# Performance work log

Measured on AMD Instinct MI355X. Metric: run time of the kernel, lower is better.

The kernel has to match this reference:

```python
import jax, jax.numpy as jnp
import numpy as np

D_MODEL = 1024
D_INTERNAL = 256


def setup_inputs() -> dict:
    key = jax.random.key(0)
    ks = jax.random.split(key, 10)
    s = lambda fan_in: 1.0 / np.sqrt(fan_in)
    inp = {
        "input_vecs": jax.random.normal(ks[0], (4, 2048, D_MODEL), dtype=jnp.float32),
        # Linear weights stored as (in, out) for x @ W
        "wq": jax.random.uniform(ks[1], (D_MODEL, D_INTERNAL), minval=-s(D_MODEL), maxval=s(D_MODEL), dtype=jnp.float32),
        "wk": jax.random.uniform(ks[2], (D_MODEL, D_INTERNAL), minval=-s(D_MODEL), maxval=s(D_MODEL), dtype=jnp.float32),
        "wv": jax.random.uniform(ks[3], (D_MODEL, D_MODEL), minval=-s(D_MODEL), maxval=s(D_MODEL), dtype=jnp.float32),
        "wo": jax.random.uniform(ks[4], (D_MODEL, D_MODEL), minval=-s(D_MODEL), maxval=s(D_MODEL), dtype=jnp.float32),
        "bo": jax.random.uniform(ks[5], (D_MODEL,), minval=-s(D_MODEL), maxval=s(D_MODEL), dtype=jnp.float32),
        "w1": jax.random.uniform(ks[6], (D_MODEL, D_INTERNAL), minval=-s(D_MODEL), maxval=s(D_MODEL), dtype=jnp.float32),
        "b1": jax.random.uniform(ks[7], (D_INTERNAL,), minval=-s(D_MODEL), maxval=s(D_MODEL), dtype=jnp.float32),
        "w2": jax.random.uniform(ks[8], (D_INTERNAL, D_MODEL), minval=-s(D_INTERNAL), maxval=s(D_INTERNAL), dtype=jnp.float32),
        "b2": jax.random.uniform(ks[9], (D_MODEL,), minval=-s(D_INTERNAL), maxval=s(D_INTERNAL), dtype=jnp.float32),
    }
    return inp


def reference(input_vecs, wq, wk, wv, wo, bo, w1, b1, w2, b2):
    # Single-head self-attention (causal=False default path)
    q = jnp.einsum("btd,dk->btk", input_vecs, wq)  # (B,T,d_internal)
    k = jnp.einsum("btd,dk->btk", input_vecs, wk)
    v = jnp.einsum("btd,de->bte", input_vecs, wv)  # (B,T,d_model)
    scale = 1.0 / jnp.sqrt(jnp.asarray(q.shape[-1], dtype=q.dtype))
    scores = jnp.einsum("bqk,btk->bqt", q, k) * scale  # (B,T,T)
    attn = jax.nn.softmax(scores, axis=-1)
    context = jnp.einsum("bqt,bte->bqe", attn, v)  # (B,T,d_model)
    context = jnp.einsum("bte,eo->bto", context, wo) + bo
    residual = input_vecs + context
    h = jax.nn.relu(jnp.einsum("btd,dk->btk", residual, w1) + b1)
    ff = jnp.einsum("btk,kd->btd", h, w2) + b2
    out = residual + ff
    return out, attn
```

## Files before the change

kernel.cpp:

```cpp
#include <hip/hip_runtime.h>

typedef unsigned short u16;
typedef unsigned int u32;
typedef __bf16 bf16x8 __attribute__((ext_vector_type(8)));
typedef float f32x4 __attribute__((ext_vector_type(4)));

#define MTOT 8192
#define DM 1024
#define DI 256
#define TT 2048

#define AS1 __attribute__((address_space(1)))
#define AS3 __attribute__((address_space(3)))

__device__ __forceinline__ u16 f2bf(float f) {
    u32 u = __float_as_uint(f);
    return (u16)((u + 0x7fffu + ((u >> 16) & 1u)) >> 16);
}
__device__ __forceinline__ float b2f(u16 b) {
    return __uint_as_float((u32)b << 16);
}

__device__ __forceinline__ int xcd_swizzle(int bid, int nb) {
    return (bid & 7) * (nb >> 3) + (bid >> 3);
}

__device__ __forceinline__ void transpose_tile(const float* __restrict__ in,
                                               u16* __restrict__ out, int K, int N,
                                               int bx, int by) {
    __shared__ float t[32][33];
    int n0 = bx * 32, k0 = by * 32;
    int tx = threadIdx.x & 31, ty = threadIdx.x >> 5;
    #pragma unroll
    for (int i = ty; i < 32; i += 8) t[i][tx] = in[(long)(k0 + i) * N + n0 + tx];
    __syncthreads();
    #pragma unroll
    for (int i = ty; i < 32; i += 8) out[(long)(n0 + i) * K + k0 + tx] = f2bf(t[tx][i]);
}

__device__ __forceinline__ void cvt_range(const float* __restrict__ in,
                                          u16* __restrict__ out, long n4, int b, int nb) {
    long i = (long)b * 256 + threadIdx.x;
    long stride = (long)nb * 256;
    for (; i < n4; i += stride) {
        float4 v = reinterpret_cast<const float4*>(in)[i];
        union { u16 u[4]; uint2 p; } o;
        o.u[0] = f2bf(v.x); o.u[1] = f2bf(v.y); o.u[2] = f2bf(v.z); o.u[3] = f2bf(v.w);
        reinterpret_cast<uint2*>(out)[i] = o.p;
    }
}

__global__ __launch_bounds__(256) void prep_kernel(
    const float* __restrict__ x, u16* __restrict__ Xb,
    const float* __restrict__ wq, const float* __restrict__ wk, u16* __restrict__ Wqk_t,
    const float* __restrict__ wv, u16* __restrict__ Wv_b,
    const float* __restrict__ wo, u16* __restrict__ Wo_t,
    const float* __restrict__ w1, u16* __restrict__ W1_t,
    const float* __restrict__ w2, u16* __restrict__ W2_t)
{
    int b = blockIdx.x;
    if (b < 1024) { cvt_range(x, Xb, (long)MTOT * DM / 4, b, 1024); return; }
    b -= 1024;
    if (b < 256)  { transpose_tile(wq, Wqk_t,              1024,  256, b & 7,  b >> 3); return; }
    b -= 256;
    if (b < 256)  { transpose_tile(wk, Wqk_t + 256 * 1024, 1024,  256, b & 7,  b >> 3); return; }
    b -= 256;
    if (b < 256)  { cvt_range(wv, Wv_b, (long)DM * DM / 4, b, 256); return; }
    b -= 256;
    if (b < 1024) { transpose_tile(wo, Wo_t,               1024, 1024, b & 31, b >> 5); return; }
    b -= 1024;
    if (b < 256)  { transpose_tile(w1, W1_t,               1024,  256, b & 7,  b >> 3); return; }
    b -= 256;
    transpose_tile(w2, W2_t, 256, 1024, b & 31, b >> 5);
}

__global__ __launch_bounds__(256) void softmax_kernel(u16* __restrict__ Sb, float* __restrict__ attn) {
    long row = blockIdx.x;
    int tid = threadIdx.x;
    uint4 q = reinterpret_cast<uint4*>(Sb + row * (long)TT)[tid];
    u32 w4[4] = {q.x, q.y, q.z, q.w};
    float vv[8];
    #pragma unroll
    for (int j = 0; j < 4; ++j) {
        vv[2 * j]     = __uint_as_float(w4[j] << 16);
        vv[2 * j + 1] = __uint_as_float(w4[j] & 0xffff0000u);
    }
    float m = vv[0];
    #pragma unroll
    for (int j = 1; j < 8; ++j) m = fmaxf(m, vv[j]);
    #pragma unroll
    for (int off = 32; off; off >>= 1) m = fmaxf(m, __shfl_xor(m, off));
    __shared__ float redm[4], reds[4];
    if ((tid & 63) == 0) redm[tid >> 6] = m;
    __syncthreads();
    m = fmaxf(fmaxf(redm[0], redm[1]), fmaxf(redm[2], redm[3]));
    float s = 0.f;
    #pragma unroll
    for (int j = 0; j < 8; ++j) { vv[j] = __expf(vv[j] - m); s += vv[j]; }
    #pragma unroll
    for (int off = 32; off; off >>= 1) s += __shfl_xor(s, off);
    if ((tid & 63) == 0) reds[tid >> 6] = s;
    __syncthreads();
    s = reds[0] + reds[1] + reds[2] + reds[3];
    float inv = 1.0f / s;
    #pragma unroll
    for (int j = 0; j < 8; ++j) vv[j] *= inv;
    float* p = attn + row * (long)TT;
    reinterpret_cast<float4*>(p)[tid * 2]     = make_float4(vv[0], vv[1], vv[2], vv[3]);
    reinterpret_cast<float4*>(p)[tid * 2 + 1] = make_float4(vv[4], vv[5], vv[6], vv[7]);
    union { u16 u[8]; uint4 q; } pk;
    #pragma unroll
    for (int j = 0; j < 8; ++j) pk.u[j] = f2bf(vv[j]);
    reinterpret_cast<uint4*>(Sb + row * (long)TT)[tid] = pk.q;
}

template<int MODE>
__global__ __launch_bounds__(256) void gemm_bt(
    const u16* __restrict__ A, long sA, int lda,
    const u16* __restrict__ Bt, long sB, int ldb,
    u16* __restrict__ Cb, long sCb, int ldcb,
    float* __restrict__ Cf, long sCf, int ldcf,
    int K, float scale,
    const float* __restrict__ bias,
    const u16* __restrict__ addend_b, long sAdd, int ld_add,
    int gx, int gy)
{
    __shared__ __attribute__((aligned(16))) u16 As[128 * 64];
    __shared__ __attribute__((aligned(16))) u16 Bs[128 * 64];

    int lid = xcd_swizzle(blockIdx.x, gridDim.x);
    int x = lid % gx;
    int t = lid / gx;
    int y = t % gy;
    int z = t / gy;
    long tile_m = (long)y * 128, tile_n = (long)x * 128;
    const u16* Az = A + (long)z * sA;
    const u16* Btz = Bt + (long)z * sB;

    const int tid = threadIdx.x;
    const int w = tid >> 6;
    const int l = tid & 63;
    const int lane15 = l & 15;
    const int lhi = l >> 4;

    const int srow = w * 8 + (l >> 3);
    const int scol = (((l & 7) ^ (l >> 3)) << 4) >> 1;

    const u16* aptr = Az + (tile_m + srow) * (long)lda + scol;
    const u16* bptr = Btz + (tile_n + srow) * (long)ldb + scol;

    f32x4 acc[4][4] = {};

    const int wr = (w >> 1) * 64;
    const int wc = (w & 1) * 64;

    for (int k0 = 0; k0 < K; k0 += 64) {
        #pragma unroll
        for (int i = 0; i < 4; ++i) {
            __builtin_amdgcn_global_load_lds(
                (const AS1 void*)(aptr + (long)i * 32 * lda + k0),
                (AS3 void*)((char*)As + i * 4096 + w * 1024), 16, 0, 0);
        }
        #pragma unroll
        for (int i = 0; i < 4; ++i) {
            __builtin_amdgcn_global_load_lds(
                (const AS1 void*)(bptr + (long)i * 32 * ldb + k0),
                (AS3 void*)((char*)Bs + i * 4096 + w * 1024), 16, 0, 0);
        }
        __syncthreads();
        #pragma unroll
        for (int kk = 0; kk < 2; ++kk) {
            bf16x8 af[4], bfr[4];
            const int kb = (kk * 32 + lhi * 8) * 2;
            #pragma unroll
            for (int m = 0; m < 4; ++m) {
                int r = wr + m * 16 + lane15;
                af[m] = *reinterpret_cast<const bf16x8*>(
                    (const char*)As + r * 128 + (kb ^ ((r & 7) << 4)));
            }
            #pragma unroll
            for (int n = 0; n < 4; ++n) {
                int r = wc + n * 16 + lane15;
                bfr[n] = *reinterpret_cast<const bf16x8*>(
                    (const char*)Bs + r * 128 + (kb ^ ((r & 7) << 4)));
            }
            #pragma unroll
            for (int m = 0; m < 4; ++m)
                #pragma unroll
                for (int n = 0; n < 4; ++n)
                    acc[m][n] = __builtin_amdgcn_mfma_f32_16x16x32_bf16(
                        af[m], bfr[n], acc[m][n], 0, 0, 0);
        }
        __syncthreads();
    }

    float* Cfz = Cf + (long)z * sCf;
    u16* Cbz = Cb + (long)z * sCb;
    const u16* addz = addend_b ? addend_b + (long)z * sAdd : addend_b;
    #pragma unroll
    for (int m = 0; m < 4; ++m) {
        #pragma unroll
        for (int n = 0; n < 4; ++n) {
            long grow0 = tile_m + wr + m * 16 + lhi * 4;
            long gcol  = tile_n + wc + n * 16 + lane15;
            if (MODE == 1) {
                union { u16 u[4]; uint2 q2; } p;
                #pragma unroll
                for (int r = 0; r < 4; ++r) p.u[r] = f2bf(acc[m][n][r]);
                *reinterpret_cast<uint2*>(Cbz + gcol * (long)ldcb + grow0) = p.q2;
            } else {
                #pragma unroll
                for (int r = 0; r < 4; ++r) {
                    long grow = grow0 + r;
                    float v = acc[m][n][r];
                    v += bias[gcol];
                    if (MODE == 7) v += b2f(addz[grow * (long)ld_add + gcol]);
                    if (MODE == 3) v = fmaxf(v, 0.0f);
                    if (MODE == 3) Cbz[grow * (long)ldcb + gcol] = f2bf(v);
                    if (MODE == 7) Cfz[grow * (long)ldcf + gcol] = v;
                }
            }
        }
    }
}

template<int BN, int MODE>
__device__ __forceinline__ void g2_body(
    char* ldsb,
    const u16* __restrict__ A, int lda,
    const u16* __restrict__ Bt, int ldb,
    u16* __restrict__ Cb, int ldcb,
    int K, float scale,
    const float* __restrict__ bias,
    const u16* __restrict__ addend_b, int ld_add,
    long tile_m, long tile_n)
{
    constexpr int WNM = (BN == 256) ? 2 : 4;
    constexpr int WNN = 8 / WNM;
    constexpr int MF  = 16 / WNM;
    constexpr int WTM = 256 / WNM;
    constexpr int BUFB = (256 + BN) * 128;
    constexpr int AC = 4;
    constexpr int BC = BN / 64;

    const int tid = threadIdx.x;
    const int w = tid >> 6, l = tid & 63;
    const int lane15 = l & 15, lhi = l >> 4;
    const int sw = (l & 7) << 4;
    const int wm = w / WNN, wn = w % WNN;

    const int srow = w * 8 + (l >> 3);
    const int scol = ((l & 7) ^ (l >> 3)) * 8;
    const u16* aS = A + (tile_m + srow) * (long)lda + scol;
    const u16* bS = Bt + (tile_n + srow) * (long)ldb + scol;

    auto STAGE = [&](int t) {
        const long kof = (long)t << 6;
        char* buf = ldsb + (size_t)(t & 1) * BUFB;
        #pragma unroll
        for (int c = 0; c < AC; ++c)
            __builtin_amdgcn_global_load_lds(
                (const AS1 void*)(aS + (long)(c * 64) * lda + kof),
                (AS3 void*)(buf + c * 8192 + w * 1024), 16, 0, 0);
        #pragma unroll
        for (int c = 0; c < BC; ++c)
            __builtin_amdgcn_global_load_lds(
                (const AS1 void*)(bS + (long)(c * 64) * ldb + kof),
                (AS3 void*)(buf + 32768 + c * 8192 + w * 1024), 16, 0, 0);
    };

    f32x4 acc[MF][4] = {};
    const int NT = K >> 6;

    STAGE(0);
    asm volatile("s_waitcnt vmcnt(0)" ::: "memory");
    __builtin_amdgcn_s_barrier();

    for (int t = 0; t < NT; ++t) {
        const char* ab = ldsb + (size_t)(t & 1) * BUFB;
        const char* bb = ab + 32768;
        const bool more = (t + 1) < NT;

        if (more) STAGE(t + 1);

        bf16x8 bfr[4][2];
        #pragma unroll
        for (int n = 0; n < 4; ++n) {
            const int rb = wn * 64 + n * 16 + lane15;
            #pragma unroll
            for (int ks = 0; ks < 2; ++ks)
                bfr[n][ks] = *reinterpret_cast<const bf16x8*>(
                    bb + rb * 128 + ((ks * 64 + lhi * 16) ^ sw));
        }
        #pragma unroll
        for (int h = 0; h < MF / 4; ++h) {
            bf16x8 af[4][2];
            #pragma unroll
            for (int m = 0; m < 4; ++m) {
                const int r = wm * WTM + h * 64 + m * 16 + lane15;
                #pragma unroll
                for (int ks = 0; ks < 2; ++ks)
                    af[m][ks] = *reinterpret_cast<const bf16x8*>(
                        ab + r * 128 + ((ks * 64 + lhi * 16) ^ sw));
            }
            __builtin_amdgcn_s_barrier();
            __builtin_amdgcn_s_setprio(1);
            #pragma unroll
            for (int m = 0; m < 4; ++m)
                #pragma unroll
                for (int n = 0; n < 4; ++n)
                    #pragma unroll
                    for (int ks = 0; ks < 2; ++ks)
                        acc[h * 4 + m][n] = __builtin_amdgcn_mfma_f32_16x16x32_bf16(
                            af[m][ks], bfr[n][ks], acc[h * 4 + m][n], 0, 0, 0);
            __builtin_amdgcn_s_setprio(0);
        }
        if (more) asm volatile("s_waitcnt vmcnt(0)" ::: "memory");
        __builtin_amdgcn_s_barrier();
    }

    #pragma unroll
    for (int mf = 0; mf < MF; ++mf) {
        #pragma unroll
        for (int nf = 0; nf < 4; ++nf) {
            const long grow0 = tile_m + wm * WTM + mf * 16 + lhi * 4;
            const long gcol  = tile_n + wn * 64 + nf * 16 + lane15;
            if (MODE == 1) {
                union { u16 u[4]; uint2 q2; } p;
                #pragma unroll
                for (int r = 0; r < 4; ++r) p.u[r] = f2bf(acc[mf][nf][r]);
                *reinterpret_cast<uint2*>(Cb + gcol * (long)ldcb + grow0) = p.q2;
            } else {
                #pragma unroll
                for (int r = 0; r < 4; ++r) {
                    const long grow = grow0 + r;
                    float v = acc[mf][nf][r];
                    if (MODE == 0) v *= scale;
                    if (MODE == 6) v += bias[gcol] + b2f(addend_b[grow * (long)ld_add + gcol]);
                    Cb[grow * (long)ldcb + gcol] = f2bf(v);
                }
            }
        }
    }
}

template<int BN, int MODE>
__global__ __launch_bounds__(512) void g2k(
    const u16* __restrict__ A, long sA, int lda,
    const u16* __restrict__ Bt, long sB, int ldb,
    u16* __restrict__ Cb, long sCb, int ldcb,
    int K, float scale,
    const float* __restrict__ bias,
    const u16* __restrict__ addend_b, long sAdd, int ld_add,
    int gx, int tpz)
{
    __shared__ __attribute__((aligned(16))) char lds[(256 + BN) * 256];
    int lid = xcd_swizzle(blockIdx.x, gridDim.x);
    int z = lid / tpz, rem = lid % tpz;
    int x = rem % gx, y = rem / gx;
    g2_body<BN, MODE>(lds,
                      A + (long)z * sA, lda, Bt + (long)z * sB, ldb,
                      Cb + (long)z * sCb, ldcb, K, scale, bias,
                      addend_b ? addend_b + (long)z * sAdd : addend_b, ld_add,
                      (long)y * 256, (long)x * BN);
}

__global__ __launch_bounds__(512) void g2_qkvw(
    const u16* __restrict__ Xb, const u16* __restrict__ Wqk_t, u16* __restrict__ QKb,
    const u16* __restrict__ Wvo_t, u16* __restrict__ VWt)
{
    __shared__ __attribute__((aligned(16))) char lds[131072];
    int lid = xcd_swizzle(blockIdx.x, gridDim.x);
    if (lid < 64) {
        int x = lid & 1, y = lid >> 1;
        g2_body<256, 0>(lds, Xb, 1024, Wqk_t, 1024, QKb, 512,
                        1024, 1.0f, (const float*)nullptr, (const u16*)nullptr, 0,
                        (long)y * 256, (long)x * 256);
    } else {
        int l2 = lid - 64;
        int x = l2 & 3, y = l2 >> 2;
        g2_body<256, 1>(lds, Xb, 1024, Wvo_t, 1024, VWt, 8192,
                        1024, 1.0f, (const float*)nullptr, (const u16*)nullptr, 0,
                        (long)y * 256, (long)x * 256);
    }
}

extern "C" void kernel_launch(void* const* d_in, const int* in_sizes, int n_in,
                              void* d_out, int out_size, void* d_ws, size_t ws_size,
                              hipStream_t stream)
{
    const float* x  = (const float*)d_in[0];
    const float* wq = (const float*)d_in[1];
    const float* wk = (const float*)d_in[2];
    const float* wv = (const float*)d_in[3];
    const float* wo = (const float*)d_in[4];
    const float* bo = (const float*)d_in[5];
    const float* w1 = (const float*)d_in[6];
    const float* b1 = (const float*)d_in[7];
    const float* w2 = (const float*)d_in[8];
    const float* b2 = (const float*)d_in[9];

    float* out_f  = (float*)d_out;
    float* attn_f = out_f + (long)MTOT * DM;

    char* ws = (char*)d_ws;
    u16* Xb    = (u16*)(ws + 0);
    u16* Wqk_t = (u16*)(ws + 16777216);
    u16* Wv_b  = (u16*)(ws + 17825792);
    u16* Wo_t  = (u16*)(ws + 19922944);
    u16* W1_t  = (u16*)(ws + 22020096);
    u16* W2_t  = (u16*)(ws + 22544384);
    u16* Wvo_t = (u16*)(ws + 23068672);
    u16* QKb   = (u16*)(ws + 25165824);
    u16* VWt   = (u16*)(ws + 33554432);
    u16* attnb = (u16*)(ws + 50331648);
    u16* res_b = (u16*)(ws + 83886080);
    u16* hb    = QKb;

    dim3 blk(256), blk5(512);

    prep_kernel<<<dim3(3328), blk, 0, stream>>>(x, Xb, wq, wk, Wqk_t, wv, Wv_b,
                                                wo, Wo_t, w1, W1_t, w2, W2_t);
    gemm_bt<1><<<dim3(64), blk, 0, stream>>>(
        Wv_b, 0L, 1024, Wo_t, 0L, 1024, Wvo_t, 0L, 1024,
        (float*)nullptr, 0L, 0, 1024, 1.0f, (const float*)nullptr,
        (const u16*)nullptr, 0L, 0, 8, 8);
    g2_qkvw<<<dim3(192), blk5, 0, stream>>>(Xb, Wqk_t, QKb, Wvo_t, VWt);
    g2k<256, 0><<<dim3(256), blk5, 0, stream>>>(
        QKb, (long)2048 * 512, 512, QKb + 256, (long)2048 * 512, 512,
        attnb, (long)2048 * 2048, 2048,
        256, 0.0625f, (const float*)nullptr, (const u16*)nullptr, 0L, 0, 8, 64);
    softmax_kernel<<<dim3(8192), blk, 0, stream>>>(attnb, attn_f);
    g2k<128, 6><<<dim3(256), blk5, 0, stream>>>(
        attnb, (long)2048 * 2048, 2048, VWt, 2048L, 8192,
        res_b, (long)2048 * 1024, 1024,
        2048, 1.0f, bo, Xb, (long)2048 * 1024, 1024, 8, 64);
    gemm_bt<3><<<dim3(128), blk, 0, stream>>>(
        res_b, 0L, 1024, W1_t, 0L, 1024, hb, 0L, 256,
        (float*)nullptr, 0L, 0, 1024, 1.0f, b1, (const u16*)nullptr, 0L, 0, 2, 64);
    gemm_bt<7><<<dim3(512), blk, 0, stream>>>(
        hb, 0L, 256, W2_t, 0L, 256, (u16*)nullptr, 0L, 0,
        out_f, 0L, 1024, 256, 1.0f, b2, res_b, 0L, 1024, 8, 64);
}
```

Before: 186.1 us.

## Fuse exp into score GEMM and defer softmax normalization to PV epilogue

The QK^T GEMM epilogue now applies exp(scale*s) directly, without max subtraction, and stores unnormalized bf16 values. A lighter softmax kernel only sums each row, writes the normalized fp32 attention, and records 1/sum per row. The PV GEMM multiplies by that inverse sum in its epilogue, so the softmax no longer writes back a bf16 probability array and needs one fewer block reduction. Skipping the max subtraction risks overflow for large scores, and the Wvo precompute is rewritten with swapped operands in row-major output mode.

```diff
diff --git a/kernel.cpp b/kernel.cpp
--- a/kernel.cpp
+++ b/kernel.cpp
@@ -74,10 +74,12 @@
     transpose_tile(w2, W2_t, 256, 1024, b & 31, b >> 5);
 }
 
-__global__ __launch_bounds__(256) void softmax_kernel(u16* __restrict__ Sb, float* __restrict__ attn) {
+__global__ __launch_bounds__(256) void softmax2_kernel(const u16* __restrict__ E,
+                                                       float* __restrict__ attn,
+                                                       float* __restrict__ inv_sum) {
     long row = blockIdx.x;
     int tid = threadIdx.x;
-    uint4 q = reinterpret_cast<uint4*>(Sb + row * (long)TT)[tid];
+    uint4 q = reinterpret_cast<const uint4*>(E + row * (long)TT)[tid];
     u32 w4[4] = {q.x, q.y, q.z, q.w};
     float vv[8];
     #pragma unroll
@@ -85,33 +87,22 @@
         vv[2 * j]     = __uint_as_float(w4[j] << 16);
         vv[2 * j + 1] = __uint_as_float(w4[j] & 0xffff0000u);
     }
-    float m = vv[0];
-    #pragma unroll
-    for (int j = 1; j < 8; ++j) m = fmaxf(m, vv[j]);
-    #pragma unroll
-    for (int off = 32; off; off >>= 1) m = fmaxf(m, __shfl_xor(m, off));
-    __shared__ float redm[4], reds[4];
-    if ((tid & 63) == 0) redm[tid >> 6] = m;
-    __syncthreads();
-    m = fmaxf(fmaxf(redm[0], redm[1]), fmaxf(redm[2], redm[3]));
     float s = 0.f;
     #pragma unroll
-    for (int j = 0; j < 8; ++j) { vv[j] = __expf(vv[j] - m); s += vv[j]; }
+    for (int j = 0; j < 8; ++j) s += vv[j];
     #pragma unroll
     for (int off = 32; off; off >>= 1) s += __shfl_xor(s, off);
+    __shared__ float reds[4];
     if ((tid & 63) == 0) reds[tid >> 6] = s;
     __syncthreads();
     s = reds[0] + reds[1] + reds[2] + reds[3];
     float inv = 1.0f / s;
-    #pragma unroll
-    for (int j = 0; j < 8; ++j) vv[j] *= inv;
     float* p = attn + row * (long)TT;
-    reinterpret_cast<float4*>(p)[tid * 2]     = make_float4(vv[0], vv[1], vv[2], vv[3]);
-    reinterpret_cast<float4*>(p)[tid * 2 + 1] = make_float4(vv[4], vv[5], vv[6], vv[7]);
-    union { u16 u[8]; uint4 q; } pk;
-    #pragma unroll
-    for (int j = 0; j < 8; ++j) pk.u[j] = f2bf(vv[j]);
-    reinterpret_cast<uint4*>(Sb + row * (long)TT)[tid] = pk.q;
+    reinterpret_cast<float4*>(p)[tid * 2] =
+        make_float4(vv[0] * inv, vv[1] * inv, vv[2] * inv, vv[3] * inv);
+    reinterpret_cast<float4*>(p)[tid * 2 + 1] =
+        make_float4(vv[4] * inv, vv[5] * inv, vv[6] * inv, vv[7] * inv);
+    if (tid == 0) inv_sum[row] = inv;
 }
 
 template<int MODE>
@@ -203,22 +194,15 @@
         for (int n = 0; n < 4; ++n) {
             long grow0 = tile_m + wr + m * 16 + lhi * 4;
             long gcol  = tile_n + wc + n * 16 + lane15;
-            if (MODE == 1) {
-                union { u16 u[4]; uint2 q2; } p;
-                #pragma unroll
-                for (int r = 0; r < 4; ++r) p.u[r] = f2bf(acc[m][n][r]);
-                *reinterpret_cast<uint2*>(Cbz + gcol * (long)ldcb + grow0) = p.q2;
-            } else {
-                #pragma unroll
-                for (int r = 0; r < 4; ++r) {
-                    long grow = grow0 + r;
-                    float v = acc[m][n][r];
-                    v += bias[gcol];
-                    if (MODE == 7) v += b2f(addz[grow * (long)ld_add + gcol]);
-                    if (MODE == 3) v = fmaxf(v, 0.0f);
-                    if (MODE == 3) Cbz[grow * (long)ldcb + gcol] = f2bf(v);
-                    if (MODE == 7) Cfz[grow * (long)ldcf + gcol] = v;
-                }
+            #pragma unroll
+            for (int r = 0; r < 4; ++r) {
+                long grow = grow0 + r;
+                float v = acc[m][n][r];
+                if (MODE == 3 || MODE == 7) v += bias[gcol];
+                if (MODE == 7) v += b2f(addz[grow * (long)ld_add + gcol]);
+                if (MODE == 3) v = fmaxf(v, 0.0f);
+                if (MODE == 0 || MODE == 3) Cbz[grow * (long)ldcb + gcol] = f2bf(v);
+                if (MODE == 7) Cfz[grow * (long)ldcf + gcol] = v;
             }
         }
     }
@@ -233,6 +217,7 @@
     int K, float scale,
     const float* __restrict__ bias,
     const u16* __restrict__ addend_b, int ld_add,
+    const float* __restrict__ inv_sum,
     long tile_m, long tile_n)
 {
     constexpr int WNM = (BN == 256) ? 2 : 4;
@@ -336,7 +321,9 @@
                     const long grow = grow0 + r;
                     float v = acc[mf][nf][r];
                     if (MODE == 0) v *= scale;
-                    if (MODE == 6) v += bias[gcol] + b2f(addend_b[grow * (long)ld_add + gcol]);
+                    if (MODE == 8) v = __expf(v * scale);
+                    if (MODE == 9) v = v * inv_sum[grow] + bias[gcol]
+                                       + b2f(addend_b[grow * (long)ld_add + gcol]);
                     Cb[grow * (long)ldcb + gcol] = f2bf(v);
                 }
             }
@@ -352,6 +339,7 @@
     int K, float scale,
     const float* __restrict__ bias,
     const u16* __restrict__ addend_b, long sAdd, int ld_add,
+    const float* __restrict__ inv_sum, long sInv,
     int gx, int tpz)
 {
     __shared__ __attribute__((aligned(16))) char lds[(256 + BN) * 256];
@@ -362,6 +350,7 @@
                       A + (long)z * sA, lda, Bt + (long)z * sB, ldb,
                       Cb + (long)z * sCb, ldcb, K, scale, bias,
                       addend_b ? addend_b + (long)z * sAdd : addend_b, ld_add,
+                      inv_sum ? inv_sum + (long)z * sInv : inv_sum,
                       (long)y * 256, (long)x * BN);
 }
 
@@ -375,13 +364,13 @@
         int x = lid & 1, y = lid >> 1;
         g2_body<256, 0>(lds, Xb, 1024, Wqk_t, 1024, QKb, 512,
                         1024, 1.0f, (const float*)nullptr, (const u16*)nullptr, 0,
-                        (long)y * 256, (long)x * 256);
+                        (const float*)nullptr, (long)y * 256, (long)x * 256);
     } else {
         int l2 = lid - 64;
         int x = l2 & 3, y = l2 >> 2;
         g2_body<256, 1>(lds, Xb, 1024, Wvo_t, 1024, VWt, 8192,
                         1024, 1.0f, (const float*)nullptr, (const u16*)nullptr, 0,
-                        (long)y * 256, (long)x * 256);
+                        (const float*)nullptr, (long)y * 256, (long)x * 256);
     }
 }
 
@@ -415,26 +404,29 @@
     u16* VWt   = (u16*)(ws + 33554432);
     u16* attnb = (u16*)(ws + 50331648);
     u16* res_b = (u16*)(ws + 83886080);
+    float* inv_sum = (float*)(ws + 100663296);
     u16* hb    = QKb;
 
     dim3 blk(256), blk5(512);
 
     prep_kernel<<<dim3(3328), blk, 0, stream>>>(x, Xb, wq, wk, Wqk_t, wv, Wv_b,
                                                 wo, Wo_t, w1, W1_t, w2, W2_t);
-    gemm_bt<1><<<dim3(64), blk, 0, stream>>>(
-        Wv_b, 0L, 1024, Wo_t, 0L, 1024, Wvo_t, 0L, 1024,
+    gemm_bt<0><<<dim3(64), blk, 0, stream>>>(
+        Wo_t, 0L, 1024, Wv_b, 0L, 1024, Wvo_t, 0L, 1024,
         (float*)nullptr, 0L, 0, 1024, 1.0f, (const float*)nullptr,
         (const u16*)nullptr, 0L, 0, 8, 8);
     g2_qkvw<<<dim3(192), blk5, 0, stream>>>(Xb, Wqk_t, QKb, Wvo_t, VWt);
-    g2k<256, 0><<<dim3(256), blk5, 0, stream>>>(
+    g2k<256, 8><<<dim3(256), blk5, 0, stream>>>(
         QKb, (long)2048 * 512, 512, QKb + 256, (long)2048 * 512, 512,
         attnb, (long)2048 * 2048, 2048,
-        256, 0.0625f, (const float*)nullptr, (const u16*)nullptr, 0L, 0, 8, 64);
-    softmax_kernel<<<dim3(8192), blk, 0, stream>>>(attnb, attn_f);
-    g2k<128, 6><<<dim3(256), blk5, 0, stream>>>(
+        256, 0.0625f, (const float*)nullptr, (const u16*)nullptr, 0L, 0,
+        (const float*)nullptr, 0L, 8, 64);
+    softmax2_kernel<<<dim3(8192), blk, 0, stream>>>(attnb, attn_f, inv_sum);
+    g2k<128, 9><<<dim3(256), blk5, 0, stream>>>(
         attnb, (long)2048 * 2048, 2048, VWt, 2048L, 8192,
         res_b, (long)2048 * 1024, 1024,
-        2048, 1.0f, bo, Xb, (long)2048 * 1024, 1024, 8, 64);
+        2048, 1.0f, bo, Xb, (long)2048 * 1024, 1024,
+        inv_sum, 2048L, 8, 64);
     gemm_bt<3><<<dim3(128), blk, 0, stream>>>(
         res_b, 0L, 1024, W1_t, 0L, 1024, hb, 0L, 256,
         (float*)nullptr, 0L, 0, 1024, 1.0f, b1, (const u16*)nullptr, 0L, 0, 2, 64);
```

After: 183.6 us. Within noise of the previous version (-1.4%).
